# Performance work log

Hardware: AMD Instinct MI355X
Metric: run time of the kernel (lower is better)

## Reference

```python
import jax, jax.numpy as jnp
import numpy as np

NUM_VARS = 10000
NUM_CLAUSES = 100000
K = 3  # literals per clause (3-SAT)
BATCH = 256


def setup_inputs() -> dict:
    key = jax.random.key(0)
    k1, k2, k3 = jax.random.split(key, 3)
    # fuzzy truth assignments in [0,1): [num_vars, batch]
    input = jax.random.uniform(k1, (NUM_VARS, BATCH), dtype=jnp.float32)
    # clause-literal incidence: variable index and negation flag per slot
    lit_idx = jax.random.randint(k2, (NUM_CLAUSES, K), 0, NUM_VARS, dtype=jnp.int64)
    lit_neg = jax.random.randint(k3, (NUM_CLAUSES, K), 0, 2, dtype=jnp.int64)
    return {"input": input, "lit_idx": lit_idx, "lit_neg": lit_neg}


def reference(input, lit_idx, lit_neg):
    # Gather literal values per clause slot: [num_clauses, K, batch]
    vals = input[lit_idx]
    # Goedel negation for negated literals: x -> 1 - x
    vals = jnp.where((lit_neg == 1)[:, :, None], 1.0 - vals, vals)
    # Fuzzy disjunction (Goedel = max) within each clause: [num_clauses, batch]
    clause_vals = jnp.max(vals, axis=1)
    # Fuzzy conjunction (Goedel = min) across clauses: [batch]
    return jnp.min(clause_vals, axis=0)
```

## Files before the change

kernel.cpp:

```cpp
#include <hip/hip_runtime.h>
#include <hip/hip_fp16.h>

#define NUM_VARS    10000
#define NUM_CLAUSES 100000
#define BATCH       256

typedef __attribute__((ext_vector_type(4))) _Float16 half4_t;
typedef __attribute__((ext_vector_type(2))) _Float16 half2_t;
typedef __attribute__((ext_vector_type(4))) float    float4_t;

__global__ __launch_bounds__(256) void fuzzy_convert_init(
    const float4_t* __restrict__ in,
    half4_t*        __restrict__ out16,
    float*          __restrict__ out)
{
    if (blockIdx.x == 0 && threadIdx.x < BATCH)
        out[threadIdx.x] = __uint_as_float(0x7F800000u);

    const int n4 = NUM_VARS * BATCH / 4;
    for (int i = blockIdx.x * blockDim.x + threadIdx.x; i < n4;
         i += gridDim.x * blockDim.x) {
        float4_t v = in[i];
        half4_t h;
        h.x = (_Float16)v.x;
        h.y = (_Float16)v.y;
        h.z = (_Float16)v.z;
        h.w = (_Float16)v.w;
        out16[i] = h;
    }
}

__global__ __launch_bounds__(512, 4) void fuzzy_cnf_kernel(
    const half2_t* __restrict__ input16,
    const int*     __restrict__ lit_idx,
    const int*     __restrict__ lit_neg,
    float*         __restrict__ out)
{
    const int wave = threadIdx.x >> 6;
    const int lane = threadIdx.x & 63;
    const int xcd  = blockIdx.x & 7;
    const int half = (xcd >= 4) ? 1 : 0;
    const int halfBlock   = ((blockIdx.x >> 3) << 2) | (xcd & 3);
    const int gwave       = halfBlock * 8 + wave;
    const int total_waves = 4096;
    const int colBase     = half * 64;

    float2 acc = make_float2(1e30f, 1e30f);

    #pragma unroll 4
    for (int c = gwave; c < NUM_CLAUSES; c += total_waves) {
        const int base = c * 3;
        const int i0 = __builtin_amdgcn_readfirstlane(lit_idx[base + 0]);
        const int i1 = __builtin_amdgcn_readfirstlane(lit_idx[base + 1]);
        const int i2 = __builtin_amdgcn_readfirstlane(lit_idx[base + 2]);
        const float n0 = (float)__builtin_amdgcn_readfirstlane(lit_neg[base + 0]);
        const float n1 = (float)__builtin_amdgcn_readfirstlane(lit_neg[base + 1]);
        const float n2 = (float)__builtin_amdgcn_readfirstlane(lit_neg[base + 2]);

        const half2_t h0 = input16[i0 * 128 + colBase + lane];
        const half2_t h1 = input16[i1 * 128 + colBase + lane];
        const half2_t h2 = input16[i2 * 128 + colBase + lane];

        float2 m;
        m.x = fmaxf(fmaxf(fabsf((float)h0.x - n0), fabsf((float)h1.x - n1)), fabsf((float)h2.x - n2));
        m.y = fmaxf(fmaxf(fabsf((float)h0.y - n0), fabsf((float)h1.y - n1)), fabsf((float)h2.y - n2));

        acc.x = fminf(acc.x, m.x);
        acc.y = fminf(acc.y, m.y);
    }

    __shared__ float sm[8][128];
    sm[wave][lane * 2 + 0] = acc.x;
    sm[wave][lane * 2 + 1] = acc.y;
    __syncthreads();

    const int t = threadIdx.x;
    if (t < 128) {
        float m = sm[0][t];
        #pragma unroll
        for (int w = 1; w < 8; ++w) m = fminf(m, sm[w][t]);
        atomicMin((unsigned int*)out + half * 128 + t, __float_as_uint(m));
    }
}

extern "C" void kernel_launch(void* const* d_in, const int* in_sizes, int n_in,
                              void* d_out, int out_size, void* d_ws, size_t ws_size,
                              hipStream_t stream) {
    const float* input   = (const float*)d_in[0];
    const int*   lit_idx = (const int*)d_in[1];
    const int*   lit_neg = (const int*)d_in[2];
    float*       out     = (float*)d_out;

    half4_t* input16 = (half4_t*)d_ws;

    fuzzy_convert_init<<<1024, 256, 0, stream>>>((const float4_t*)input, input16, out);
    fuzzy_cnf_kernel<<<1024, 512, 0, stream>>>((const half2_t*)input16, lit_idx, lit_neg, out);
}
```

Baseline: 91.27 us.

## Drop fp16 conversion pass and gather fp32 inputs directly with quarter-batch XCD split

Removes the separate kernel that converted the whole input to fp16, leaving only a one-block init of the output, and gathers fp32 values directly from the original input. The batch is now split into four 64-column quarters mapped to XCD pairs, so each wave handles one float per lane and half as many total waves share the clause range. This saves a full read and write pass over the input and one kernel's work. In exchange, each gathered row segment is twice as wide in bytes, and each wave walks twice as many clauses.

Result: slower. 100.2 us (+9.8%).

```diff
diff --git a/kernel.cpp b/kernel.cpp
--- a/kernel.cpp
+++ b/kernel.cpp
@@ -1,51 +1,30 @@
 #include <hip/hip_runtime.h>
-#include <hip/hip_fp16.h>
 
 #define NUM_VARS    10000
 #define NUM_CLAUSES 100000
 #define BATCH       256
 
-typedef __attribute__((ext_vector_type(4))) _Float16 half4_t;
-typedef __attribute__((ext_vector_type(2))) _Float16 half2_t;
-typedef __attribute__((ext_vector_type(4))) float    float4_t;
-
-__global__ __launch_bounds__(256) void fuzzy_convert_init(
-    const float4_t* __restrict__ in,
-    half4_t*        __restrict__ out16,
-    float*          __restrict__ out)
+__global__ __launch_bounds__(256) void fuzzy_init_out(float* __restrict__ out)
 {
-    if (blockIdx.x == 0 && threadIdx.x < BATCH)
-        out[threadIdx.x] = __uint_as_float(0x7F800000u);
-
-    const int n4 = NUM_VARS * BATCH / 4;
-    for (int i = blockIdx.x * blockDim.x + threadIdx.x; i < n4;
-         i += gridDim.x * blockDim.x) {
-        float4_t v = in[i];
-        half4_t h;
-        h.x = (_Float16)v.x;
-        h.y = (_Float16)v.y;
-        h.z = (_Float16)v.z;
-        h.w = (_Float16)v.w;
-        out16[i] = h;
-    }
+    out[threadIdx.x] = __uint_as_float(0x7F800000u);
 }
 
-__global__ __launch_bounds__(512, 4) void fuzzy_cnf_kernel(
-    const half2_t* __restrict__ input16,
-    const int*     __restrict__ lit_idx,
-    const int*     __restrict__ lit_neg,
-    float*         __restrict__ out)
+__global__ __launch_bounds__(512, 4) void fuzzy_cnf_fp32(
+    const float* __restrict__ input,
+    const int*   __restrict__ lit_idx,
+    const int*   __restrict__ lit_neg,
+    float*       __restrict__ out)
 {
     const int wave = threadIdx.x >> 6;
     const int lane = threadIdx.x & 63;
     const int xcd  = blockIdx.x & 7;
-    const int half = (xcd >= 4) ? 1 : 0;
-    const int halfBlock   = ((blockIdx.x >> 3) << 2) | (xcd & 3);
-    const int gwave       = halfBlock * 8 + wave;
-    const int total_waves = 4096;
-    const int colBase     = half * 64;
+    const int quarter = xcd >> 1;
+    const int qBlock  = ((blockIdx.x >> 3) << 1) | (xcd & 1);
+    const int gwave   = qBlock * 8 + wave;
+    const int total_waves = 2048;
+    const int colBase = quarter * 64;
 
-    float2 acc = make_float2(1e30f, 1e30f);
+    float acc = 1e30f;
 
     #pragma unroll 4
     for (int c = gwave; c < NUM_CLAUSES; c += total_waves) {
@@ -57,29 +36,24 @@
         const float n1 = (float)__builtin_amdgcn_readfirstlane(lit_neg[base + 1]);
         const float n2 = (float)__builtin_amdgcn_readfirstlane(lit_neg[base + 2]);
 
-        const half2_t h0 = input16[i0 * 128 + colBase + lane];
-        const half2_t h1 = input16[i1 * 128 + colBase + lane];
-        const half2_t h2 = input16[i2 * 128 + colBase + lane];
+        const float x0 = input[(i0 << 8) + colBase + lane];
+        const float x1 = input[(i1 << 8) + colBase + lane];
+        const float x2 = input[(i2 << 8) + colBase + lane];
 
-        float2 m;
-        m.x = fmaxf(fmaxf(fabsf((float)h0.x - n0), fabsf((float)h1.x - n1)), fabsf((float)h2.x - n2));
-        m.y = fmaxf(fmaxf(fabsf((float)h0.y - n0), fabsf((float)h1.y - n1)), fabsf((float)h2.y - n2));
-
-        acc.x = fminf(acc.x, m.x);
-        acc.y = fminf(acc.y, m.y);
+        const float m = fmaxf(fmaxf(fabsf(x0 - n0), fabsf(x1 - n1)),
+                              fabsf(x2 - n2));
+        acc = fminf(acc, m);
     }
 
-    __shared__ float sm[8][128];
-    sm[wave][lane * 2 + 0] = acc.x;
-    sm[wave][lane * 2 + 1] = acc.y;
+    __shared__ float sm[8][64];
+    sm[wave][lane] = acc;
     __syncthreads();
 
-    const int t = threadIdx.x;
-    if (t < 128) {
-        float m = sm[0][t];
+    if (threadIdx.x < 64) {
+        float m = sm[0][threadIdx.x];
         #pragma unroll
-        for (int w = 1; w < 8; ++w) m = fminf(m, sm[w][t]);
-        atomicMin((unsigned int*)out + half * 128 + t, __float_as_uint(m));
+        for (int w = 1; w < 8; ++w) m = fminf(m, sm[w][threadIdx.x]);
+        atomicMin((unsigned int*)out + colBase + threadIdx.x, __float_as_uint(m));
     }
 }
 
@@ -91,8 +65,8 @@
     const int*   lit_neg = (const int*)d_in[2];
     float*       out     = (float*)d_out;
 
-    half4_t* input16 = (half4_t*)d_ws;
+    (void)d_ws; (void)ws_size;
 
-    fuzzy_convert_init<<<1024, 256, 0, stream>>>((const float4_t*)input, input16, out);
-    fuzzy_cnf_kernel<<<1024, 512, 0, stream>>>((const half2_t*)input16, lit_idx, lit_neg, out);
+    fuzzy_init_out<<<1, 256, 0, stream>>>(out);
+    fuzzy_cnf_fp32<<<1024, 512, 0, stream>>>(input, lit_idx, lit_neg, out);
 }
```

## Batch 8 clauses per wave iteration with packed fp16 min/max math

Applied to the files above, without the earlier changes.

Each wave now handles a contiguous chunk of 8 clauses per iteration. It loads all 24 indices and negation flags up front, then issues all 24 gathers before computing, which raises memory-level parallelism and cuts per-clause loop overhead. Negation is done as a packed half2 FMA and the max/min reductions run in fp16, replacing the fp32 converts. The launch bound asks for higher occupancy, which could cause register spills. Indices are no longer readfirstlane'd, so they may stay in vector registers, and the fp16 accumulator changes precision slightly.

Measured after the change: 79.36 us. -13.0%, faster.

```diff
diff --git a/kernel.cpp b/kernel.cpp
--- a/kernel.cpp
+++ b/kernel.cpp
@@ -4,10 +4,26 @@
 #define NUM_VARS    10000
 #define NUM_CLAUSES 100000
 #define BATCH       256
+#define CPI         8
+#define NCHUNK      (NUM_CLAUSES / CPI)
+#define WAVES_H     4096
 
 typedef __attribute__((ext_vector_type(4))) _Float16 half4_t;
 typedef __attribute__((ext_vector_type(2))) _Float16 half2_t;
 typedef __attribute__((ext_vector_type(4))) float    float4_t;
+
+static __device__ __forceinline__ half2_t h2max(half2_t a, half2_t b) {
+    half2_t r;
+    r.x = (a.x > b.x) ? a.x : b.x;
+    r.y = (a.y > b.y) ? a.y : b.y;
+    return r;
+}
+static __device__ __forceinline__ half2_t h2min(half2_t a, half2_t b) {
+    half2_t r;
+    r.x = (a.x < b.x) ? a.x : b.x;
+    r.y = (a.y < b.y) ? a.y : b.y;
+    return r;
+}
 
 __global__ __launch_bounds__(256) void fuzzy_convert_init(
     const float4_t* __restrict__ in,
@@ -22,56 +38,64 @@
          i += gridDim.x * blockDim.x) {
         float4_t v = in[i];
         half4_t h;
-        h.x = (_Float16)v.x;
-        h.y = (_Float16)v.y;
-        h.z = (_Float16)v.z;
-        h.w = (_Float16)v.w;
+        h.x = (_Float16)v.x;  h.y = (_Float16)v.y;
+        h.z = (_Float16)v.z;  h.w = (_Float16)v.w;
         out16[i] = h;
     }
 }
 
-__global__ __launch_bounds__(512, 4) void fuzzy_cnf_kernel(
+__global__ __launch_bounds__(512, 8) void fuzzy_cnf_fp16(
     const half2_t* __restrict__ input16,
     const int*     __restrict__ lit_idx,
     const int*     __restrict__ lit_neg,
     float*         __restrict__ out)
 {
-    const int wave = threadIdx.x >> 6;
-    const int lane = threadIdx.x & 63;
-    const int xcd  = blockIdx.x & 7;
-    const int half = (xcd >= 4) ? 1 : 0;
-    const int halfBlock   = ((blockIdx.x >> 3) << 2) | (xcd & 3);
-    const int gwave       = halfBlock * 8 + wave;
-    const int total_waves = 4096;
-    const int colBase     = half * 64;
+    const int wave   = threadIdx.x >> 6;
+    const int lane   = threadIdx.x & 63;
+    const int xcd    = blockIdx.x & 7;
+    const int half   = (xcd >= 4) ? 1 : 0;
+    const int hBlock = ((blockIdx.x >> 3) << 2) | (xcd & 3);
+    const int gwave  = __builtin_amdgcn_readfirstlane(hBlock * 8 + wave);
+    const int coff   = half * 64 + lane;
 
-    float2 acc = make_float2(1e30f, 1e30f);
+    half2_t acc;
+    acc.x = (_Float16)30000.0f;  acc.y = (_Float16)30000.0f;
 
-    #pragma unroll 4
-    for (int c = gwave; c < NUM_CLAUSES; c += total_waves) {
-        const int base = c * 3;
-        const int i0 = __builtin_amdgcn_readfirstlane(lit_idx[base + 0]);
-        const int i1 = __builtin_amdgcn_readfirstlane(lit_idx[base + 1]);
-        const int i2 = __builtin_amdgcn_readfirstlane(lit_idx[base + 2]);
-        const float n0 = (float)__builtin_amdgcn_readfirstlane(lit_neg[base + 0]);
-        const float n1 = (float)__builtin_amdgcn_readfirstlane(lit_neg[base + 1]);
-        const float n2 = (float)__builtin_amdgcn_readfirstlane(lit_neg[base + 2]);
+    #pragma unroll 1
+    for (int ch = gwave; ch < NCHUNK; ch += WAVES_H) {
+        const int base = ch * (CPI * 3);
 
-        const half2_t h0 = input16[i0 * 128 + colBase + lane];
-        const half2_t h1 = input16[i1 * 128 + colBase + lane];
-        const half2_t h2 = input16[i2 * 128 + colBase + lane];
+        int idx[CPI * 3];
+        int neg[CPI * 3];
+        #pragma unroll
+        for (int j = 0; j < CPI * 3; ++j) idx[j] = lit_idx[base + j];
+        #pragma unroll
+        for (int j = 0; j < CPI * 3; ++j) neg[j] = lit_neg[base + j];
 
-        float2 m;
-        m.x = fmaxf(fmaxf(fabsf((float)h0.x - n0), fabsf((float)h1.x - n1)), fabsf((float)h2.x - n2));
-        m.y = fmaxf(fmaxf(fabsf((float)h0.y - n0), fabsf((float)h1.y - n1)), fabsf((float)h2.y - n2));
+        half2_t x[CPI * 3];
+        #pragma unroll
+        for (int j = 0; j < CPI * 3; ++j)
+            x[j] = input16[idx[j] * 128 + coff];
 
-        acc.x = fminf(acc.x, m.x);
-        acc.y = fminf(acc.y, m.y);
+        #pragma unroll
+        for (int q = 0; q < CPI; ++q) {
+            half2_t v[3];
+            #pragma unroll
+            for (int l = 0; l < 3; ++l) {
+                const int j = 3 * q + l;
+                const _Float16 s = neg[j] ? (_Float16)-1.0f : (_Float16)1.0f;
+                const _Float16 n = neg[j] ? (_Float16)1.0f  : (_Float16)0.0f;
+                half2_t sv; sv.x = s; sv.y = s;
+                half2_t nv; nv.x = n; nv.y = n;
+                v[l] = x[j] * sv + nv;
+            }
+            acc = h2min(acc, h2max(h2max(v[0], v[1]), v[2]));
+        }
     }
 
     __shared__ float sm[8][128];
-    sm[wave][lane * 2 + 0] = acc.x;
-    sm[wave][lane * 2 + 1] = acc.y;
+    sm[wave][lane * 2 + 0] = (float)acc.x;
+    sm[wave][lane * 2 + 1] = (float)acc.y;
     __syncthreads();
 
     const int t = threadIdx.x;
@@ -93,6 +117,8 @@
 
     half4_t* input16 = (half4_t*)d_ws;
 
-    fuzzy_convert_init<<<1024, 256, 0, stream>>>((const float4_t*)input, input16, out);
-    fuzzy_cnf_kernel<<<1024, 512, 0, stream>>>((const half2_t*)input16, lit_idx, lit_neg, out);
+    fuzzy_convert_init<<<1024, 256, 0, stream>>>((const float4_t*)input,
+                                                 input16, out);
+    fuzzy_cnf_fp16<<<1024, 512, 0, stream>>>((const half2_t*)input16,
+                                             lit_idx, lit_neg, out);
 }
```
